# Kernel tuning notes

Hardware: AMD Instinct MI355X
Metric: run time of the kernel (lower is better)

## Reference

```python
import jax, jax.numpy as jnp
import numpy as np

B, S, D, H = 4, 2048, 1024, 16
HD = D // H  # head_dim = 64


def setup_inputs() -> dict:
    key = jax.random.key(0)
    ks = jax.random.split(key, 5)
    scale = 0.02
    x = jax.random.normal(ks[0], (B, S, D), dtype=jnp.float32)
    W_qkv = jax.random.normal(ks[1], (D, 3 * D), dtype=jnp.float32) * scale
    b_qkv = jnp.zeros((3 * D,), dtype=jnp.float32)
    W_out = jax.random.normal(ks[2], (D, D), dtype=jnp.float32) * scale
    b_out = jnp.zeros((D,), dtype=jnp.float32)
    return {"x": x, "W_qkv": W_qkv, "b_qkv": b_qkv, "W_out": W_out, "b_out": b_out}


def reference(x, W_qkv, b_qkv, W_out, b_out):
    b, s, d = x.shape
    qkv = x @ W_qkv + b_qkv                      # [B,S,3D]
    q, k, v = jnp.split(qkv, 3, axis=-1)
    # [B,S,D] -> [B,H,S,hd]
    q = q.reshape(b, s, H, HD).transpose(0, 2, 1, 3)
    k = k.reshape(b, s, H, HD).transpose(0, 2, 1, 3)
    v = v.reshape(b, s, H, HD).transpose(0, 2, 1, 3)
    scores = jnp.einsum('bhqd,bhkd->bhqk', q, k) / jnp.sqrt(jnp.float32(HD))
    causal = jnp.tril(jnp.ones((s, s), dtype=bool))  # [S,S]
    scores = jnp.where(causal[None, None], scores, -jnp.inf)
    probs = jax.nn.softmax(scores, axis=-1)
    # dropout is identity in eval mode
    attn = jnp.einsum('bhqk,bhkd->bhqd', probs, v)  # [B,H,S,hd]
    attn = attn.transpose(0, 2, 1, 3).reshape(b, s, d)
    return attn @ W_out + b_out
```

## Files before the change

### kernel.cpp

```cpp
#include <hip/hip_runtime.h>


typedef short s16;
typedef __attribute__((ext_vector_type(4))) short s16x4;
typedef __attribute__((ext_vector_type(8))) short bf16x8;
typedef __attribute__((ext_vector_type(4))) float f32x4;

__device__ __forceinline__ s16 f2bf(float f) {
    union { float f; unsigned int i; } v;
    v.f = f;
    unsigned int r = v.i + 0x7fffu + ((v.i >> 16) & 1u);
    return (s16)(r >> 16);
}

__device__ __forceinline__ unsigned pack_bf16(float a, float b) {
    union { float f; unsigned u; } x, y;
    x.f = a; y.f = b;
    return __byte_perm(x.u + 0x8000u, y.u + 0x8000u, 0x7632);
}

__device__ __forceinline__ void load_lds16(const s16* g, s16* lds_base) {
    __builtin_amdgcn_global_load_lds(
        (const __attribute__((address_space(1))) void*)g,
        (__attribute__((address_space(3))) void*)lds_base, 16, 0, 0);
}

__global__ void cast_f32_bf16(const float* __restrict__ in, s16* __restrict__ out) {
    const int i = (blockIdx.x * 256 + threadIdx.x) * 4;
    const float4 f = *(const float4*)(in + i);
    s16x4 r = {f2bf(f.x), f2bf(f.y), f2bf(f.z), f2bf(f.w)};
    *(s16x4*)(out + i) = r;
}

__global__ void transpose_cast(const float* __restrict__ in,
                               s16* __restrict__ out, int R, int C) {
    __shared__ float tile[32][33];
    const int cb = blockIdx.x * 32, rb = blockIdx.y * 32;
    const int tx = threadIdx.x, ty = threadIdx.y;
#pragma unroll
    for (int i = 0; i < 32; i += 8)
        tile[ty + i][tx] = in[(size_t)(rb + ty + i) * C + cb + tx];
    __syncthreads();
#pragma unroll
    for (int i = 0; i < 32; i += 8)
        out[(size_t)(cb + ty + i) * R + rb + tx] = f2bf(tile[tx][ty + i]);
}

template <bool OUT_F32>
__global__ __launch_bounds__(256) void gemm_bt_bias(
    const s16* __restrict__ A,
    const s16* __restrict__ Bt,
    const float* __restrict__ bias,
    void* __restrict__ Cv,
    int M, int N, int K) {
    __shared__ __attribute__((aligned(16))) s16 As[128 * 32];
    __shared__ __attribute__((aligned(16))) s16 Bs[128 * 32];

    const int tid  = threadIdx.x;
    const int lane = tid & 63;
    const int wave = tid >> 6;
    const int l15  = lane & 15;
    const int quad = lane >> 4;
    const int m0 = blockIdx.y * 128;
    const int n0 = blockIdx.x * 128;
    const int wm = (wave & 1) * 64;
    const int wn = (wave >> 1) * 64;

    f32x4 acc[4][4];
#pragma unroll
    for (int i = 0; i < 4; ++i)
#pragma unroll
        for (int j = 0; j < 4; ++j)
            acc[i][j] = (f32x4){0.f, 0.f, 0.f, 0.f};

    const int r_a = tid >> 2;
    const int kp  = tid & 3;

    for (int k0 = 0; k0 < K; k0 += 32) {
        __syncthreads();
#pragma unroll
        for (int c = 0; c < 2; ++c) {
            load_lds16(A  + (size_t)(m0 + c * 64 + r_a) * K + k0 + kp * 8, As + c * 2048 + wave * 512);
            load_lds16(Bt + (size_t)(n0 + c * 64 + r_a) * K + k0 + kp * 8, Bs + c * 2048 + wave * 512);
        }
        __syncthreads();

        bf16x8 af[4], bfv[4];
#pragma unroll
        for (int mt = 0; mt < 4; ++mt)
            af[mt] = *(const bf16x8*)(As + (wm + mt * 16 + l15) * 32 + quad * 8);
#pragma unroll
        for (int nt = 0; nt < 4; ++nt)
            bfv[nt] = *(const bf16x8*)(Bs + (wn + nt * 16 + l15) * 32 + quad * 8);
#pragma unroll
        for (int mt = 0; mt < 4; ++mt)
#pragma unroll
            for (int nt = 0; nt < 4; ++nt)
                acc[mt][nt] = __builtin_amdgcn_mfma_f32_16x16x32_bf16(af[mt], bfv[nt], acc[mt][nt], 0, 0, 0);
    }

#pragma unroll
    for (int nt = 0; nt < 4; ++nt) {
        const int col = n0 + wn + nt * 16 + l15;
        const float bv = bias[col];
#pragma unroll
        for (int mt = 0; mt < 4; ++mt) {
            const int rowb = m0 + wm + mt * 16 + quad * 4;
#pragma unroll
            for (int r = 0; r < 4; ++r) {
                const float v = acc[mt][nt][r] + bv;
                if constexpr (OUT_F32)
                    ((float*)Cv)[(size_t)(rowb + r) * N + col] = v;
                else
                    ((s16*)Cv)[(size_t)(rowb + r) * N + col] = f2bf(v);
            }
        }
    }
}

__global__ __launch_bounds__(256) void attn_fwd(
    const s16* __restrict__ qkv,
    s16* __restrict__ attn) {
    __shared__ __attribute__((aligned(16))) s16 Ks[64 * 72];
    __shared__ __attribute__((aligned(16))) s16 Vt[64 * 72];
    __shared__ __attribute__((aligned(16))) s16 PT[4][32][88];

    const int tid  = threadIdx.x;
    const int lane = tid & 63;
    const int wave = tid >> 6;
    const int l15  = lane & 15;
    const int quad = lane >> 4;

    const int bid = blockIdx.x;
    const int hi  = bid >> 8;
    const int a   = bid & 3;
    const int bh  = (bid >> 2) & 63;
    const int qbase = a * 2 + (hi >> 1);
    const int qt  = (hi & 1) ? 15 - qbase : qbase;

    const size_t rowbase = (size_t)(bh >> 4) * 2048;
    const int hoff = (bh & 15) * 64;
    const int kp  = tid >> 3;
    const int p_s = tid & 7;
    const int kg  = kp >> 2;

    const float C2 = 0.18033688011112042f;
    const float M2 = 12.0f;

    const int wq = qt * 128 + wave * 32;

    bf16x8 qf[2][2];
#pragma unroll
    for (int qs = 0; qs < 2; ++qs)
#pragma unroll
        for (int ks = 0; ks < 2; ++ks)
            qf[qs][ks] = *(const bf16x8*)(qkv + (rowbase + wq + qs * 16 + l15) * 3072 + hoff + ks * 32 + quad * 8);

    float l_lane[2] = {0.f, 0.f};
    f32x4 o[2][4];
#pragma unroll
    for (int qs = 0; qs < 2; ++qs)
#pragma unroll
        for (int hs = 0; hs < 4; ++hs)
            o[qs][hs] = (f32x4){0.f, 0.f, 0.f, 0.f};

    const int nkt = qt * 2 + 2;
    bf16x8 kv[2], vv[2];
#pragma unroll
    for (int dk = 0; dk < 2; ++dk) {
        const s16* g = qkv + (rowbase + 2 * kp + dk) * 3072 + hoff + p_s * 8;
        kv[dk] = *(const bf16x8*)(g + 1024);
        vv[dk] = *(const bf16x8*)(g + 2048);
    }

    for (int kt = 0; kt < nkt; ++kt) {
        const int k0 = kt * 64;
        __syncthreads();
#pragma unroll
        for (int dk = 0; dk < 2; ++dk)
            *(bf16x8*)(Ks + (2 * kp + dk) * 72 + p_s * 8) = kv[dk];
#pragma unroll
        for (int j = 0; j < 8; ++j) {
            const unsigned dw = (unsigned)(unsigned short)vv[0][j] |
                                ((unsigned)(unsigned short)vv[1][j] << 16);
            *(unsigned*)(Vt + (p_s * 8 + j) * 72 + ((kg ^ p_s) << 3) + (2 * kp & 7)) = dw;
        }
        __syncthreads();

        if (kt + 1 < nkt) {
#pragma unroll
            for (int dk = 0; dk < 2; ++dk) {
                const s16* g = qkv + (rowbase + k0 + 64 + 2 * kp + dk) * 3072 + hoff + p_s * 8;
                kv[dk] = *(const bf16x8*)(g + 1024);
                vv[dk] = *(const bf16x8*)(g + 2048);
            }
        }

        if (k0 > wq + 31) continue;

        f32x4 st[2][4];
#pragma unroll
        for (int qs = 0; qs < 2; ++qs)
#pragma unroll
            for (int kb = 0; kb < 4; ++kb)
                st[qs][kb] = (f32x4){0.f, 0.f, 0.f, 0.f};
        __builtin_amdgcn_s_setprio(1);
#pragma unroll
        for (int kb = 0; kb < 4; ++kb)
#pragma unroll
            for (int ks = 0; ks < 2; ++ks) {
                const bf16x8 kf = *(const bf16x8*)(Ks + (kb * 16 + l15) * 72 + ks * 32 + quad * 8);
#pragma unroll
                for (int qs = 0; qs < 2; ++qs)
                    st[qs][kb] = __builtin_amdgcn_mfma_f32_16x16x32_bf16(kf, qf[qs][ks], st[qs][kb], 0, 0, 0);
            }
        __builtin_amdgcn_s_setprio(0);

        const bool edge = (k0 + 63 > wq);
#pragma unroll
        for (int qs = 0; qs < 2; ++qs) {
            const int q = wq + qs * 16 + l15;
#pragma unroll
            for (int kb = 0; kb < 4; ++kb) {
                float p4[4];
#pragma unroll
                for (int r = 0; r < 4; ++r) {
                    float t = fmaf(st[qs][kb][r], C2, -M2);
                    if (edge) {
                        const int key = k0 + kb * 16 + quad * 4 + r;
                        t = (key <= q) ? t : -150.f;
                    }
                    p4[r] = __builtin_amdgcn_exp2f(t);
                    l_lane[qs] += p4[r];
                }
                uint2 dd;
                dd.x = pack_bf16(p4[0], p4[1]);
                dd.y = pack_bf16(p4[2], p4[3]);
                *(uint2*)(&PT[wave][qs * 16 + l15][kb * 16 + quad * 4]) = dd;
            }
        }

        __builtin_amdgcn_s_setprio(1);
#pragma unroll
        for (int kk = 0; kk < 2; ++kk) {
            bf16x8 pf[2];
#pragma unroll
            for (int qs = 0; qs < 2; ++qs)
                pf[qs] = *(const bf16x8*)(&PT[wave][qs * 16 + l15][kk * 32 + quad * 8]);
#pragma unroll
            for (int hs = 0; hs < 4; ++hs) {
                const bf16x8 vf = *(const bf16x8*)(
                    Vt + (hs * 16 + l15) * 72 + (((kk * 4 + quad) ^ (2 * hs + (l15 >> 3))) << 3));
#pragma unroll
                for (int qs = 0; qs < 2; ++qs)
                    o[qs][hs] = __builtin_amdgcn_mfma_f32_16x16x32_bf16(vf, pf[qs], o[qs][hs], 0, 0, 0);
            }
        }
        __builtin_amdgcn_s_setprio(0);
    }

    float rl[2];
#pragma unroll
    for (int qs = 0; qs < 2; ++qs) {
        float l = l_lane[qs];
        l += __shfl_xor(l, 16);
        l += __shfl_xor(l, 32);
        rl[qs] = 1.f / l;
    }

#pragma unroll
    for (int qs = 0; qs < 2; ++qs) {
        const int q = wq + qs * 16 + l15;
#pragma unroll
        for (int hs = 0; hs < 4; ++hs) {
            uint2 dd;
            dd.x = pack_bf16(o[qs][hs][0] * rl[qs], o[qs][hs][1] * rl[qs]);
            dd.y = pack_bf16(o[qs][hs][2] * rl[qs], o[qs][hs][3] * rl[qs]);
            *(uint2*)(attn + (rowbase + q) * 1024 + hoff + hs * 16 + quad * 4) = dd;
        }
    }
}

extern "C" void kernel_launch(void* const* d_in, const int* in_sizes, int n_in,
                              void* d_out, int out_size, void* d_ws, size_t ws_size,
                              hipStream_t stream) {
    const float* x    = (const float*)d_in[0];
    const float* Wqkv = (const float*)d_in[1];
    const float* bqkv = (const float*)d_in[2];
    const float* Wout = (const float*)d_in[3];
    const float* bout = (const float*)d_in[4];
    float* out = (float*)d_out;

    s16* ws   = (s16*)d_ws;
    s16* qkv  = ws;
    s16* xba  = qkv + (size_t)8192 * 3072;
    s16* wtq  = xba + (size_t)8192 * 1024;
    s16* wto  = wtq + (size_t)3072 * 1024;

    cast_f32_bf16<<<8192, 256, 0, stream>>>(x, xba);
    transpose_cast<<<dim3(3072 / 32, 1024 / 32), dim3(32, 8), 0, stream>>>(Wqkv, wtq, 1024, 3072);
    transpose_cast<<<dim3(1024 / 32, 1024 / 32), dim3(32, 8), 0, stream>>>(Wout, wto, 1024, 1024);
    gemm_bt_bias<false><<<dim3(3072 / 128, 8192 / 128), 256, 0, stream>>>(
        xba, wtq, bqkv, qkv, 8192, 3072, 1024);
    attn_fwd<<<1024, 256, 0, stream>>>(qkv, xba);
    gemm_bt_bias<true><<<dim3(1024 / 128, 8192 / 128), 256, 0, stream>>>(
        xba, wto, bout, out, 8192, 1024, 1024);
}
```

Baseline: 270.4 us.

## Rewrite GEMM as 8-wave double-buffered 128x256 tile with swizzled LDS

Replaces the 4-wave 128x128 GEMM with an 8-wave kernel using a 128x256 tile and a K step of 64. LDS is double-buffered, and the next tile's global-to-LDS loads are issued during the MFMA phases. An XOR swizzle on LDS rows avoids bank conflicts, and s_setprio raises wave priority around the MFMA bursts. The goal is to hide memory latency and cut per-iteration barrier overhead in both projection GEMMs, at the cost of 96KB of LDS per block, which limits occupancy, and fewer blocks for the small output GEMM.

```diff
diff --git a/kernel.cpp b/kernel.cpp
--- a/kernel.cpp
+++ b/kernel.cpp
@@ -47,24 +47,34 @@
 }
 
 template <bool OUT_F32>
-__global__ __launch_bounds__(256) void gemm_bt_bias(
+__global__ __launch_bounds__(512, 2) void gemm_bt_bias_8p(
     const s16* __restrict__ A,
     const s16* __restrict__ Bt,
     const float* __restrict__ bias,
     void* __restrict__ Cv,
     int M, int N, int K) {
-    __shared__ __attribute__((aligned(16))) s16 As[128 * 32];
-    __shared__ __attribute__((aligned(16))) s16 Bs[128 * 32];
+    __shared__ __attribute__((aligned(16))) s16 As[2][128 * 64];
+    __shared__ __attribute__((aligned(16))) s16 Bs[2][256 * 64];
 
     const int tid  = threadIdx.x;
     const int lane = tid & 63;
     const int wave = tid >> 6;
     const int l15  = lane & 15;
     const int quad = lane >> 4;
+    const int wr   = wave >> 2;
+    const int wc   = wave & 3;
     const int m0 = blockIdx.y * 128;
-    const int n0 = blockIdx.x * 128;
-    const int wm = (wave & 1) * 64;
-    const int wn = (wave >> 1) * 64;
+    const int n0 = blockIdx.x * 256;
+
+    const int srow = tid >> 3;
+    const int sg   = (tid & 7) ^ (srow & 7);
+    const s16* Ag = A  + (size_t)(m0 + srow) * K + sg * 8;
+    const s16* Bg = Bt + (size_t)(n0 + srow) * K + sg * 8;
+
+#define STAGE_A8(buf, h, kt) load_lds16(Ag + (size_t)(h) * 64 * K + (size_t)(kt) * 64, \
+                                        &As[buf][(h) * 4096 + wave * 512])
+#define STAGE_B8(buf, u, kt) load_lds16(Bg + (size_t)(u) * 64 * K + (size_t)(kt) * 64, \
+                                        &Bs[buf][(u) * 4096 + wave * 512])
 
     f32x4 acc[4][4];
 #pragma unroll
@@ -73,39 +83,65 @@
         for (int j = 0; j < 4; ++j)
             acc[i][j] = (f32x4){0.f, 0.f, 0.f, 0.f};
 
-    const int r_a = tid >> 2;
-    const int kp  = tid & 3;
-
-    for (int k0 = 0; k0 < K; k0 += 32) {
-        __syncthreads();
-#pragma unroll
-        for (int c = 0; c < 2; ++c) {
-            load_lds16(A  + (size_t)(m0 + c * 64 + r_a) * K + k0 + kp * 8, As + c * 2048 + wave * 512);
-            load_lds16(Bt + (size_t)(n0 + c * 64 + r_a) * K + k0 + kp * 8, Bs + c * 2048 + wave * 512);
-        }
-        __syncthreads();
-
-        bf16x8 af[4], bfv[4];
-#pragma unroll
-        for (int mt = 0; mt < 4; ++mt)
-            af[mt] = *(const bf16x8*)(As + (wm + mt * 16 + l15) * 32 + quad * 8);
-#pragma unroll
-        for (int nt = 0; nt < 4; ++nt)
-            bfv[nt] = *(const bf16x8*)(Bs + (wn + nt * 16 + l15) * 32 + quad * 8);
-#pragma unroll
-        for (int mt = 0; mt < 4; ++mt)
-#pragma unroll
-            for (int nt = 0; nt < 4; ++nt)
-                acc[mt][nt] = __builtin_amdgcn_mfma_f32_16x16x32_bf16(af[mt], bfv[nt], acc[mt][nt], 0, 0, 0);
-    }
+    const int nk = K >> 6;
+
+    STAGE_A8(0, 0, 0); STAGE_A8(0, 1, 0);
+    STAGE_B8(0, 0, 0); STAGE_B8(0, 1, 0); STAGE_B8(0, 2, 0); STAGE_B8(0, 3, 0);
+    __syncthreads();
+
+    for (int t = 0; t < nk; ++t) {
+        const int buf  = t & 1;
+        const int nbuf = buf ^ 1;
+        const bool pre = (t + 1 < nk);
+#pragma unroll
+        for (int p = 0; p < 4; ++p) {
+            const int mh = p >> 1, nh = p & 1;
+            bf16x8 af[2][2], bfr[2][2];
+#pragma unroll
+            for (int i = 0; i < 2; ++i)
+#pragma unroll
+                for (int ks = 0; ks < 2; ++ks) {
+                    const int ar = wr * 64 + (mh * 2 + i) * 16 + l15;
+                    const int br = wc * 64 + (nh * 2 + i) * 16 + l15;
+                    const int gs = ((ks * 4 + quad) ^ (l15 & 7)) * 8;
+                    af[i][ks]  = *(const bf16x8*)(&As[buf][ar * 64 + gs]);
+                    bfr[i][ks] = *(const bf16x8*)(&Bs[buf][br * 64 + gs]);
+                }
+            if (p == 0 && pre) {
+                STAGE_A8(nbuf, 0, t + 1); STAGE_A8(nbuf, 1, t + 1);
+                STAGE_B8(nbuf, 0, t + 1);
+            }
+            if (p == 1 && pre) {
+                STAGE_B8(nbuf, 1, t + 1); STAGE_B8(nbuf, 2, t + 1);
+                STAGE_B8(nbuf, 3, t + 1);
+            }
+            __builtin_amdgcn_s_barrier();
+            __builtin_amdgcn_s_setprio(1);
+#pragma unroll
+            for (int i = 0; i < 2; ++i)
+#pragma unroll
+                for (int j = 0; j < 2; ++j)
+#pragma unroll
+                    for (int ks = 0; ks < 2; ++ks)
+                        acc[mh * 2 + i][nh * 2 + j] = __builtin_amdgcn_mfma_f32_16x16x32_bf16(
+                            af[i][ks], bfr[j][ks], acc[mh * 2 + i][nh * 2 + j], 0, 0, 0);
+            __builtin_amdgcn_s_setprio(0);
+            if (p == 3)
+                __syncthreads();
+            else
+                __builtin_amdgcn_s_barrier();
+        }
+    }
+#undef STAGE_A8
+#undef STAGE_B8
 
 #pragma unroll
     for (int nt = 0; nt < 4; ++nt) {
-        const int col = n0 + wn + nt * 16 + l15;
+        const int col = n0 + wc * 64 + nt * 16 + l15;
         const float bv = bias[col];
 #pragma unroll
         for (int mt = 0; mt < 4; ++mt) {
-            const int rowb = m0 + wm + mt * 16 + quad * 4;
+            const int rowb = m0 + wr * 64 + mt * 16 + quad * 4;
 #pragma unroll
             for (int r = 0; r < 4; ++r) {
                 const float v = acc[mt][nt][r] + bv;
@@ -300,9 +336,9 @@
     cast_f32_bf16<<<8192, 256, 0, stream>>>(x, xba);
     transpose_cast<<<dim3(3072 / 32, 1024 / 32), dim3(32, 8), 0, stream>>>(Wqkv, wtq, 1024, 3072);
     transpose_cast<<<dim3(1024 / 32, 1024 / 32), dim3(32, 8), 0, stream>>>(Wout, wto, 1024, 1024);
-    gemm_bt_bias<false><<<dim3(3072 / 128, 8192 / 128), 256, 0, stream>>>(
+    gemm_bt_bias_8p<false><<<dim3(3072 / 256, 8192 / 128), 512, 0, stream>>>(
         xba, wtq, bqkv, qkv, 8192, 3072, 1024);
     attn_fwd<<<1024, 256, 0, stream>>>(qkv, xba);
-    gemm_bt_bias<true><<<dim3(1024 / 128, 8192 / 128), 256, 0, stream>>>(
+    gemm_bt_bias_8p<true><<<dim3(1024 / 256, 8192 / 128), 512, 0, stream>>>(
         xba, wto, bout, out, 8192, 1024, 1024);
 }
```

Result: no change. 269.0 us (-0.5%).

## Rewrite GEMMs with triple-buffered async LDS pipeline, larger tiles, swizzles

Applied to the files above, without the earlier changes.

Replaces the simple two-barrier GEMM with a templated 512-thread kernel that stages tiles three-deep using async global-to-LDS loads and vmcnt waits, so loads overlap MFMA work. It also uses larger block tiles (256x384 for QKV, 256x128 for the output projection), an XOR-swizzled LDS layout to avoid bank conflicts, block-id swizzling for L2 locality, and setprio around the MFMA section. The two weight transpose launches are merged into one grid. The cost is more LDS and registers per block, and fewer blocks (256) to fill the device.

```diff
diff --git a/kernel.cpp b/kernel.cpp
--- a/kernel.cpp
+++ b/kernel.cpp
@@ -25,6 +25,13 @@
         (__attribute__((address_space(3))) void*)lds_base, 16, 0, 0);
 }
 
+template <int N>
+__device__ __forceinline__ void waitcnt_vm() {
+    if constexpr (N == 0)      asm volatile("s_waitcnt vmcnt(0)" ::: "memory");
+    else if constexpr (N == 3) asm volatile("s_waitcnt vmcnt(3)" ::: "memory");
+    else if constexpr (N == 5) asm volatile("s_waitcnt vmcnt(5)" ::: "memory");
+}
+
 __global__ void cast_f32_bf16(const float* __restrict__ in, s16* __restrict__ out) {
     const int i = (blockIdx.x * 256 + threadIdx.x) * 4;
     const float4 f = *(const float4*)(in + i);
@@ -32,9 +39,18 @@
     *(s16x4*)(out + i) = r;
 }
 
-__global__ void transpose_cast(const float* __restrict__ in,
-                               s16* __restrict__ out, int R, int C) {
+__global__ void transpose_cast2(const float* __restrict__ Wq, s16* __restrict__ oq,
+                                const float* __restrict__ Wo, s16* __restrict__ oo) {
     __shared__ float tile[32][33];
+    const float* in;
+    s16* out;
+    int C;
+    if (blockIdx.z == 0) { in = Wq; out = oq; C = 3072; }
+    else {
+        if (blockIdx.x >= 32) return;
+        in = Wo; out = oo; C = 1024;
+    }
+    const int R = 1024;
     const int cb = blockIdx.x * 32, rb = blockIdx.y * 32;
     const int tx = threadIdx.x, ty = threadIdx.y;
 #pragma unroll
@@ -46,73 +62,113 @@
         out[(size_t)(cb + ty + i) * R + rb + tx] = f2bf(tile[tx][ty + i]);
 }
 
-template <bool OUT_F32>
-__global__ __launch_bounds__(256) void gemm_bt_bias(
+template <bool OUT_F32, int ACH, int BCH, int NWN_L2, int MF, int NF>
+__global__ __launch_bounds__(512, 2) void gemm_tb(
     const s16* __restrict__ A,
     const s16* __restrict__ Bt,
     const float* __restrict__ bias,
     void* __restrict__ Cv,
-    int M, int N, int K) {
-    __shared__ __attribute__((aligned(16))) s16 As[128 * 32];
-    __shared__ __attribute__((aligned(16))) s16 Bs[128 * 32];
+    int M, int N, int K, int gx) {
+    constexpr int NWN   = 1 << NWN_L2;
+    constexpr int LOADS = ACH + BCH;
+    constexpr int ABUF  = ACH * 4096;
+    constexpr int BBUF  = BCH * 4096;
+    constexpr int BM = ACH * 128, BN = BCH * 128;
+    static_assert(MF * 16 * (8 / NWN) == BM, "M geometry");
+    static_assert(NF * 16 * NWN == BN, "N geometry");
+    __shared__ __attribute__((aligned(16))) s16 As[3 * ABUF];
+    __shared__ __attribute__((aligned(16))) s16 Bs[3 * BBUF];
 
     const int tid  = threadIdx.x;
     const int lane = tid & 63;
     const int wave = tid >> 6;
     const int l15  = lane & 15;
     const int quad = lane >> 4;
-    const int m0 = blockIdx.y * 128;
-    const int n0 = blockIdx.x * 128;
-    const int wm = (wave & 1) * 64;
-    const int wn = (wave >> 1) * 64;
-
-    f32x4 acc[4][4];
-#pragma unroll
-    for (int i = 0; i < 4; ++i)
-#pragma unroll
-        for (int j = 0; j < 4; ++j)
+    const int wr   = wave >> NWN_L2;
+    const int wc   = wave & (NWN - 1);
+
+    const int cpx = (int)gridDim.x >> 3;
+    const int bid = (int)blockIdx.x;
+    const int swz = (bid & 7) * cpx + (bid >> 3);
+    const int m0 = (swz / gx) * BM;
+    const int n0 = (swz % gx) * BN;
+
+    const int sr  = tid >> 2;
+    const int gl  = tid & 3;
+    const int gsw = gl ^ ((sr >> 1) & 3);
+    const s16* Ag = A  + (size_t)(m0 + sr) * K + gsw * 8;
+    const s16* Bg = Bt + (size_t)(n0 + sr) * K + gsw * 8;
+
+#define STG(bufi, kt) do {                                                          \
+    _Pragma("unroll")                                                               \
+    for (int c = 0; c < ACH; ++c)                                                   \
+        load_lds16(Ag + (size_t)c * 128 * K + (size_t)(kt) * 32,                    \
+                   &As[(bufi) * ABUF + c * 4096 + wave * 512]);                     \
+    _Pragma("unroll")                                                               \
+    for (int c = 0; c < BCH; ++c)                                                   \
+        load_lds16(Bg + (size_t)c * 128 * K + (size_t)(kt) * 32,                    \
+                   &Bs[(bufi) * BBUF + c * 4096 + wave * 512]); } while (0)
+
+    f32x4 acc[MF][NF];
+#pragma unroll
+    for (int i = 0; i < MF; ++i)
+#pragma unroll
+        for (int j = 0; j < NF; ++j)
             acc[i][j] = (f32x4){0.f, 0.f, 0.f, 0.f};
 
-    const int r_a = tid >> 2;
-    const int kp  = tid & 3;
-
-    for (int k0 = 0; k0 < K; k0 += 32) {
-        __syncthreads();
-#pragma unroll
-        for (int c = 0; c < 2; ++c) {
-            load_lds16(A  + (size_t)(m0 + c * 64 + r_a) * K + k0 + kp * 8, As + c * 2048 + wave * 512);
-            load_lds16(Bt + (size_t)(n0 + c * 64 + r_a) * K + k0 + kp * 8, Bs + c * 2048 + wave * 512);
-        }
-        __syncthreads();
-
-        bf16x8 af[4], bfv[4];
-#pragma unroll
-        for (int mt = 0; mt < 4; ++mt)
-            af[mt] = *(const bf16x8*)(As + (wm + mt * 16 + l15) * 32 + quad * 8);
-#pragma unroll
-        for (int nt = 0; nt < 4; ++nt)
-            bfv[nt] = *(const bf16x8*)(Bs + (wn + nt * 16 + l15) * 32 + quad * 8);
-#pragma unroll
-        for (int mt = 0; mt < 4; ++mt)
-#pragma unroll
-            for (int nt = 0; nt < 4; ++nt)
-                acc[mt][nt] = __builtin_amdgcn_mfma_f32_16x16x32_bf16(af[mt], bfv[nt], acc[mt][nt], 0, 0, 0);
-    }
-
-#pragma unroll
-    for (int nt = 0; nt < 4; ++nt) {
-        const int col = n0 + wn + nt * 16 + l15;
-        const float bv = bias[col];
-#pragma unroll
-        for (int mt = 0; mt < 4; ++mt) {
-            const int rowb = m0 + wm + mt * 16 + quad * 4;
-#pragma unroll
-            for (int r = 0; r < 4; ++r) {
-                const float v = acc[mt][nt][r] + bv;
+    const int nk = K >> 5;
+
+    STG(0, 0);
+    STG(1, 1);
+    waitcnt_vm<LOADS>();
+    __builtin_amdgcn_s_barrier();
+
+    for (int t = 0; t < nk; ++t) {
+        const int cur = t % 3;
+        if (t + 2 < nk) STG((t + 2) % 3, t + 2);
+
+        const s16* Ab = As + cur * ABUF;
+        const s16* Bb = Bs + cur * BBUF;
+        bf16x8 bf[NF];
+#pragma unroll
+        for (int nf = 0; nf < NF; ++nf) {
+            const int row = wc * (NF * 16) + nf * 16 + l15;
+            bf[nf] = *(const bf16x8*)(Bb + row * 32 + ((quad ^ ((row >> 1) & 3)) << 3));
+        }
+        __builtin_amdgcn_s_setprio(1);
+#pragma unroll
+        for (int mf = 0; mf < MF; ++mf) {
+            const int row = wr * (MF * 16) + mf * 16 + l15;
+            const bf16x8 af = *(const bf16x8*)(Ab + row * 32 + ((quad ^ ((row >> 1) & 3)) << 3));
+#pragma unroll
+            for (int nf = 0; nf < NF; ++nf)
+                acc[mf][nf] = __builtin_amdgcn_mfma_f32_16x16x32_bf16(af, bf[nf], acc[mf][nf], 0, 0, 0);
+        }
+        __builtin_amdgcn_s_setprio(0);
+
+        if (t + 2 < nk)      waitcnt_vm<LOADS>();
+        else if (t + 1 < nk) waitcnt_vm<0>();
+        if (t + 1 < nk) __builtin_amdgcn_s_barrier();
+    }
+#undef STG
+
+    float bv[NF];
+#pragma unroll
+    for (int nf = 0; nf < NF; ++nf)
+        bv[nf] = bias[n0 + wc * (NF * 16) + nf * 16 + l15];
+#pragma unroll
+    for (int mf = 0; mf < MF; ++mf) {
+#pragma unroll
+        for (int r = 0; r < 4; ++r) {
+            const int row = m0 + wr * (MF * 16) + mf * 16 + quad * 4 + r;
+#pragma unroll
+            for (int nf = 0; nf < NF; ++nf) {
+                const int col = n0 + wc * (NF * 16) + nf * 16 + l15;
+                const float v = acc[mf][nf][r] + bv[nf];
                 if constexpr (OUT_F32)
-                    ((float*)Cv)[(size_t)(rowb + r) * N + col] = v;
+                    ((float*)Cv)[(size_t)row * N + col] = v;
                 else
-                    ((s16*)Cv)[(size_t)(rowb + r) * N + col] = f2bf(v);
+                    ((s16*)Cv)[(size_t)row * N + col] = f2bf(v);
             }
         }
     }
@@ -298,11 +354,10 @@
     s16* wto  = wtq + (size_t)3072 * 1024;
 
     cast_f32_bf16<<<8192, 256, 0, stream>>>(x, xba);
-    transpose_cast<<<dim3(3072 / 32, 1024 / 32), dim3(32, 8), 0, stream>>>(Wqkv, wtq, 1024, 3072);
-    transpose_cast<<<dim3(1024 / 32, 1024 / 32), dim3(32, 8), 0, stream>>>(Wout, wto, 1024, 1024);
-    gemm_bt_bias<false><<<dim3(3072 / 128, 8192 / 128), 256, 0, stream>>>(
-        xba, wtq, bqkv, qkv, 8192, 3072, 1024);
+    transpose_cast2<<<dim3(96, 32, 2), dim3(32, 8), 0, stream>>>(Wqkv, wtq, Wout, wto);
+    gemm_tb<false, 2, 3, 2, 8, 6><<<256, 512, 0, stream>>>(
+        xba, wtq, bqkv, qkv, 8192, 3072, 1024, 8);
     attn_fwd<<<1024, 256, 0, stream>>>(qkv, xba);
-    gemm_bt_bias<true><<<dim3(1024 / 128, 8192 / 128), 256, 0, stream>>>(
-        xba, wto, bout, out, 8192, 1024, 1024);
-}
+    gemm_tb<true, 2, 1, 1, 4, 4><<<256, 512, 0, stream>>>(
+        xba, wto, bout, out, 8192, 1024, 1024, 8);
+}
```

Result: faster. 261.5 us (-3.3%).
